# Kernel optimization log

Measured on AMD Instinct MI355X. Metric: run time of the kernel, lower is better.

Reference implementation:

```python
import jax, jax.numpy as jnp
import numpy as np

B, N, F = 1024, 784, 1
C1, C2, H, NCLS = 32, 32, 512, 10


def setup_inputs() -> dict:
    key = jax.random.key(0)
    ks = jax.random.split(key, 10)
    x = jax.random.normal(ks[0], (B, N, F), jnp.float32)
    # dense (renormalized-style) adjacency, shared across the batch; rows roughly sum to ~1
    a = jax.random.uniform(ks[1], (N, N), jnp.float32) * (2.0 / N)
    def glorot(k, shape):
        lim = np.sqrt(6.0 / (shape[0] + shape[1])).astype(np.float32)
        return jax.random.uniform(k, shape, jnp.float32, -lim, lim)
    return {
        "x": x,
        "a": a,
        "w1": glorot(ks[2], (F, C1)),
        "b1": jnp.zeros((C1,), jnp.float32),
        "w2": glorot(ks[3], (C1, C2)),
        "b2": jnp.zeros((C2,), jnp.float32),
        "wf1": glorot(ks[4], (N * C2, H)),
        "bf1": jnp.zeros((H,), jnp.float32),
        "wf2": glorot(ks[5], (H, NCLS)),
        "bf2": jnp.zeros((NCLS,), jnp.float32),
    }


def _graph_conv(x, a, w, b):
    # Spektral GraphConv (batch mode): elu(A @ (X @ W) + b)
    xw = jnp.einsum('bnf,fc->bnc', x, w)
    agg = jnp.einsum('nm,bmc->bnc', a, xw)
    return jax.nn.elu(agg + b)


def reference(x, a, w1, b1, w2, b2, wf1, bf1, wf2, bf2):
    h = _graph_conv(x, a, w1, b1)          # [B, N, 32]
    h = _graph_conv(h, a, w2, b2)          # [B, N, 32]
    h = h.reshape(h.shape[0], -1)          # Flatten -> [B, N*32]
    h = jax.nn.relu(h @ wf1 + bf1)         # [B, 512]
    return jax.nn.softmax(h @ wf2 + bf2, axis=-1)  # [B, 10]
```

## Files before the change

### kernel.cpp

```cpp
#include <hip/hip_runtime.h>
#include <hip/hip_bf16.h>
#include <math.h>

#define BATCH 1024
#define NREAL 784
#define NPAD  896
#define C1D   32
#define C2D   32
#define HDIM  512
#define NCLS  10
#define KFC   25088

#define KS_G1 7
#define KS_FC 14

#define BM 128
#define BN 128
#define BK 32

using bf16x8  = __attribute__((ext_vector_type(8))) __bf16;
using floatx4 = __attribute__((ext_vector_type(4))) float;

__device__ __forceinline__ float elu_f(float t) {
    return t > 0.f ? t : (__expf(t) - 1.f);
}

__device__ __forceinline__ void wg_barrier_lds() {
    asm volatile("s_waitcnt lgkmcnt(0)\n\ts_barrier" ::: "memory");
}

template<int MODE>
__launch_bounds__(256)
__global__ void gemm_bt(const __hip_bfloat16* __restrict__ A, int lda,
                        const __hip_bfloat16* __restrict__ Bm, int ldb,
                        int kIters, int kPerZ, size_t sliceStride,
                        float* __restrict__ outF, int ldc,
                        __hip_bfloat16* __restrict__ outH,
                        const float* __restrict__ bias)
{
    __shared__ __align__(16) __hip_bfloat16 As[2][BM * BK];
    __shared__ __align__(16) __hip_bfloat16 Bs[2][BN * BK];

    const int tid  = threadIdx.x;
    const int lane = tid & 63;
    const int wave = tid >> 6;
    const int wi = wave >> 1, wj = wave & 1;

    const int m0 = blockIdx.y * BM;
    const int n0 = blockIdx.x * BN;
    const int kBase = blockIdx.z * kPerZ;

    const int rowInChunk = lane >> 2;
    const int kOff8 = (lane & 3) * 8;

    const __hip_bfloat16* aSrc0 = A  + (size_t)(m0 + (wave * 2 + 0) * 16 + rowInChunk) * lda + kBase + kOff8;
    const __hip_bfloat16* aSrc1 = A  + (size_t)(m0 + (wave * 2 + 1) * 16 + rowInChunk) * lda + kBase + kOff8;
    const __hip_bfloat16* bSrc0 = Bm + (size_t)(n0 + (wave * 2 + 0) * 16 + rowInChunk) * ldb + kBase + kOff8;
    const __hip_bfloat16* bSrc1 = Bm + (size_t)(n0 + (wave * 2 + 1) * 16 + rowInChunk) * ldb + kBase + kOff8;

    const int wSlot = (((lane & 3) + ((lane >> 3) & 3)) & 3) * 8;
    const int ldsW0 = (wave * 2 + 0) * 512 + rowInChunk * 32 + wSlot;
    const int ldsW1 = ldsW0 + 512;

    const int rSlot = ((((lane >> 4) + (((lane & 15) >> 1) & 3)) & 3)) * 8;
    const int rRow  = lane & 15;

    floatx4 acc[4][4];
    const floatx4 zero4 = {0.f, 0.f, 0.f, 0.f};
    #pragma unroll
    for (int i = 0; i < 4; i++)
        #pragma unroll
        for (int j = 0; j < 4; j++) acc[i][j] = zero4;

    int4 aA0, aA1, bA0, bA1;
    int4 aB0, aB1, bB0, bB1;

    aA0 = *(const int4*)aSrc0; aA1 = *(const int4*)aSrc1;
    bA0 = *(const int4*)bSrc0; bA1 = *(const int4*)bSrc1;
    aSrc0 += BK; aSrc1 += BK; bSrc0 += BK; bSrc1 += BK;
    aB0 = *(const int4*)aSrc0; aB1 = *(const int4*)aSrc1;
    bB0 = *(const int4*)bSrc0; bB1 = *(const int4*)bSrc1;
    aSrc0 += BK; aSrc1 += BK; bSrc0 += BK; bSrc1 += BK;

    *(int4*)(&As[0][ldsW0]) = aA0;
    *(int4*)(&As[0][ldsW1]) = aA1;
    *(int4*)(&Bs[0][ldsW0]) = bA0;
    *(int4*)(&Bs[0][ldsW1]) = bA1;
    wg_barrier_lds();

    for (int kt = 0; kt < kIters; kt += 2) {
        const bool more = (kt + 2 < kIters);

        {
            bf16x8 af[4], bfr[4];
            #pragma unroll
            for (int mi = 0; mi < 4; mi++)
                af[mi] = *(const bf16x8*)(&As[0][(wi * 64 + mi * 16 + rRow) * BK + rSlot]);
            #pragma unroll
            for (int nj = 0; nj < 4; nj++)
                bfr[nj] = *(const bf16x8*)(&Bs[0][(wj * 64 + nj * 16 + rRow) * BK + rSlot]);

            if (more) {
                aA0 = *(const int4*)aSrc0; aA1 = *(const int4*)aSrc1;
                bA0 = *(const int4*)bSrc0; bA1 = *(const int4*)bSrc1;
                aSrc0 += BK; aSrc1 += BK; bSrc0 += BK; bSrc1 += BK;
            }
            *(int4*)(&As[1][ldsW0]) = aB0;
            *(int4*)(&As[1][ldsW1]) = aB1;
            *(int4*)(&Bs[1][ldsW0]) = bB0;
            *(int4*)(&Bs[1][ldsW1]) = bB1;

            #pragma unroll
            for (int mi = 0; mi < 4; mi++)
                #pragma unroll
                for (int nj = 0; nj < 4; nj++)
                    acc[mi][nj] = __builtin_amdgcn_mfma_f32_16x16x32_bf16(af[mi], bfr[nj], acc[mi][nj], 0, 0, 0);

            wg_barrier_lds();
        }

        {
            bf16x8 af[4], bfr[4];
            #pragma unroll
            for (int mi = 0; mi < 4; mi++)
                af[mi] = *(const bf16x8*)(&As[1][(wi * 64 + mi * 16 + rRow) * BK + rSlot]);
            #pragma unroll
            for (int nj = 0; nj < 4; nj++)
                bfr[nj] = *(const bf16x8*)(&Bs[1][(wj * 64 + nj * 16 + rRow) * BK + rSlot]);

            if (more) {
                aB0 = *(const int4*)aSrc0; aB1 = *(const int4*)aSrc1;
                bB0 = *(const int4*)bSrc0; bB1 = *(const int4*)bSrc1;
                aSrc0 += BK; aSrc1 += BK; bSrc0 += BK; bSrc1 += BK;
                *(int4*)(&As[0][ldsW0]) = aA0;
                *(int4*)(&As[0][ldsW1]) = aA1;
                *(int4*)(&Bs[0][ldsW0]) = bA0;
                *(int4*)(&Bs[0][ldsW1]) = bA1;
            }

            #pragma unroll
            for (int mi = 0; mi < 4; mi++)
                #pragma unroll
                for (int nj = 0; nj < 4; nj++)
                    acc[mi][nj] = __builtin_amdgcn_mfma_f32_16x16x32_bf16(af[mi], bfr[nj], acc[mi][nj], 0, 0, 0);

            wg_barrier_lds();
        }
    }

    #pragma unroll
    for (int mi = 0; mi < 4; mi++) {
        #pragma unroll
        for (int nj = 0; nj < 4; nj++) {
            #pragma unroll
            for (int r = 0; r < 4; r++) {
                const int row = m0 + wi * 64 + mi * 16 + (lane >> 4) * 4 + r;
                const int col = n0 + wj * 64 + nj * 16 + (lane & 15);
                const float v = acc[mi][nj][r];
                if (MODE == 1) {
                    if (row < NREAL) {
                        const int c = col & 31, b = col >> 5;
                        const float t = elu_f(v + bias[c]);
                        outH[(size_t)b * KFC + row * 32 + c] = __float2bfloat16(t);
                    }
                } else {
                    outF[(size_t)blockIdx.z * sliceStride + (size_t)row * ldc + col] = v;
                }
            }
        }
    }
}

__global__ void convX(const float* __restrict__ x, __hip_bfloat16* __restrict__ Xbf) {
    const int idx = blockIdx.x * 256 + threadIdx.x;
    if (idx >= BATCH * NPAD) return;
    const int m = idx % NPAD, b = idx / NPAD;
    const float v = (m < NREAL) ? x[(size_t)b * NREAL + m] : 0.f;
    Xbf[idx] = __float2bfloat16(v);
}

__global__ void convA(const float* __restrict__ a, __hip_bfloat16* __restrict__ Abf) {
    const int idx = blockIdx.x * 256 + threadIdx.x;
    if (idx >= NPAD * NPAD) return;
    const int m = idx % NPAD, n = idx / NPAD;
    const float v = (m < NREAL && n < NREAL) ? a[(size_t)n * NREAL + m] : 0.f;
    Abf[idx] = __float2bfloat16(v);
}

__global__ void convW(const float* __restrict__ wf1, __hip_bfloat16* __restrict__ Wt) {
    __shared__ float tile[32][33];
    const int k0 = blockIdx.x * 32, h0 = blockIdx.y * 32;
    const int tx = threadIdx.x, ty = threadIdx.y;
    #pragma unroll
    for (int i = 0; i < 4; i++)
        tile[ty * 4 + i][tx] = wf1[(size_t)(k0 + ty * 4 + i) * HDIM + h0 + tx];
    __syncthreads();
    #pragma unroll
    for (int i = 0; i < 4; i++)
        Wt[(size_t)(h0 + ty * 4 + i) * KFC + k0 + tx] = __float2bfloat16(tile[tx][ty * 4 + i]);
}

__global__ void layer1_fuse(const float* __restrict__ Ypart,
                            const float* __restrict__ w1, const float* __restrict__ b1,
                            const float* __restrict__ w2,
                            __hip_bfloat16* __restrict__ Tt)
{
    __shared__ __align__(16) float sW2[C1D * C2D];
    __shared__ float sw1[C1D], sb1[C1D];
    const int tid = threadIdx.x;
    for (int i = tid; i < C1D * C2D; i += 128) sW2[i] = w2[i];
    if (tid < C1D) { sw1[tid] = w1[tid]; sb1[tid] = b1[tid]; }
    __syncthreads();

    const int m = blockIdx.x * 128 + tid;
    const int b = blockIdx.y;
    float y = 0.f;
    #pragma unroll
    for (int z = 0; z < KS_G1; z++)
        y += Ypart[(size_t)z * (BATCH * NPAD) + (size_t)b * NPAD + m];

    float h[C1D];
    #pragma unroll
    for (int c1 = 0; c1 < C1D; c1++) h[c1] = elu_f(y * sw1[c1] + sb1[c1]);

    float4 t4[8];
    #pragma unroll
    for (int q = 0; q < 8; q++) t4[q] = make_float4(0.f, 0.f, 0.f, 0.f);
    #pragma unroll
    for (int c1 = 0; c1 < C1D; c1++) {
        const float hv = h[c1];
        const float4* row = (const float4*)(sW2 + c1 * C2D);
        #pragma unroll
        for (int q = 0; q < 8; q++) {
            const float4 w = row[q];
            t4[q].x += hv * w.x; t4[q].y += hv * w.y;
            t4[q].z += hv * w.z; t4[q].w += hv * w.w;
        }
    }
    const float* tf = (const float*)t4;
    #pragma unroll
    for (int c = 0; c < C2D; c++)
        Tt[((size_t)(b * 32 + c)) * NPAD + m] = __float2bfloat16(tf[c]);
}

__global__ void fc2_softmax(const float* __restrict__ part, const float* __restrict__ bf1,
                            const float* __restrict__ wf2, const float* __restrict__ bf2,
                            float* __restrict__ out)
{
    __shared__ float sW[HDIM * NCLS];
    __shared__ float sb[NCLS];
    const int tid = threadIdx.x;
    for (int i = tid; i < HDIM * NCLS; i += 256) sW[i] = wf2[i];
    if (tid < NCLS) sb[tid] = bf2[tid];
    __syncthreads();

    const int lane = tid & 63, wave = tid >> 6;
    const int b = blockIdx.x * 4 + wave;

    float acc[NCLS];
    #pragma unroll
    for (int c = 0; c < NCLS; c++) acc[c] = 0.f;
    #pragma unroll
    for (int q = 0; q < 8; q++) {
        const int h = q * 64 + lane;
        float hv = bf1[h];
        #pragma unroll
        for (int z = 0; z < KS_FC; z++)
            hv += part[(size_t)z * (BATCH * HDIM) + (size_t)b * HDIM + h];
        hv = hv > 0.f ? hv : 0.f;
        #pragma unroll
        for (int c = 0; c < NCLS; c++) acc[c] += hv * sW[h * NCLS + c];
    }
    #pragma unroll
    for (int c = 0; c < NCLS; c++) {
        #pragma unroll
        for (int off = 32; off >= 1; off >>= 1) acc[c] += __shfl_down(acc[c], off);
    }
    if (lane == 0) {
        float mx = -1e30f;
        #pragma unroll
        for (int c = 0; c < NCLS; c++) { acc[c] += sb[c]; mx = fmaxf(mx, acc[c]); }
        float e[NCLS], s = 0.f;
        #pragma unroll
        for (int c = 0; c < NCLS; c++) { e[c] = __expf(acc[c] - mx); s += e[c]; }
        const float inv = 1.f / s;
        #pragma unroll
        for (int c = 0; c < NCLS; c++) out[(size_t)b * NCLS + c] = e[c] * inv;
    }
}

extern "C" void kernel_launch(void* const* d_in, const int* in_sizes, int n_in,
                              void* d_out, int out_size, void* d_ws, size_t ws_size,
                              hipStream_t stream)
{
    const float* x   = (const float*)d_in[0];
    const float* a   = (const float*)d_in[1];
    const float* w1  = (const float*)d_in[2];
    const float* b1  = (const float*)d_in[3];
    const float* w2  = (const float*)d_in[4];
    const float* b2  = (const float*)d_in[5];
    const float* wf1 = (const float*)d_in[6];
    const float* bf1 = (const float*)d_in[7];
    const float* wf2 = (const float*)d_in[8];
    const float* bf2 = (const float*)d_in[9];
    float* out = (float*)d_out;

    char* ws = (char*)d_ws;
    __hip_bfloat16* h2f  = (__hip_bfloat16*)(ws + 0);
    float*          Ypart= (float*)(ws + 0);
    __hip_bfloat16* Tt   = (__hip_bfloat16*)(ws + 51380224);
    __hip_bfloat16* Wt   = (__hip_bfloat16*)(ws + 51380224);
    float*          part = (float*)(ws + 77070336);
    __hip_bfloat16* Abf  = (__hip_bfloat16*)(ws + 110100480);
    __hip_bfloat16* Xbf  = (__hip_bfloat16*)(ws + 111706112);

    convX<<<(BATCH * NPAD + 255) / 256, 256, 0, stream>>>(x, Xbf);
    convA<<<(NPAD * NPAD + 255) / 256, 256, 0, stream>>>(a, Abf);

    gemm_bt<2><<<dim3(NPAD / BN, BATCH / BM, KS_G1), 256, 0, stream>>>(
        Xbf, NPAD, Abf, NPAD, (NPAD / KS_G1) / BK, NPAD / KS_G1,
        (size_t)BATCH * NPAD, Ypart, NPAD, nullptr, nullptr);

    layer1_fuse<<<dim3(NPAD / 128, BATCH), 128, 0, stream>>>(Ypart, w1, b1, w2, Tt);

    gemm_bt<1><<<dim3((BATCH * 32) / BN, NPAD / BM, 1), 256, 0, stream>>>(
        Abf, NPAD, Tt, NPAD, NPAD / BK, 0, 0, nullptr, 0, h2f, b2);

    convW<<<dim3(KFC / 32, HDIM / 32), dim3(32, 8), 0, stream>>>(wf1, Wt);

    gemm_bt<2><<<dim3(HDIM / BN, BATCH / BM, KS_FC), 256, 0, stream>>>(
        h2f, KFC, Wt, KFC, (KFC / KS_FC) / BK, KFC / KS_FC,
        (size_t)BATCH * HDIM, part, HDIM, nullptr, nullptr);

    fc2_softmax<<<BATCH / 4, 256, 0, stream>>>(part, bf1, wf2, bf2, out);
}
```

Measured before the change: 300.1 us.

## Pre-swizzle A operands into MFMA fragment layout and load directly to registers

The A operand of every GEMM is now stored in a fragment-tiled layout (16 rows x 32 k chunks of 512 elements), so each wave loads its MFMA A fragments straight from global memory into registers and skips the LDS staging for A. A new prepXA kernel writes X and the adjacency into this layout. The layer-2 epilogue writes h2 in the same tiled layout for the FC GEMM. This halves LDS traffic and barrier-covered stores, at the cost of more register pressure, an extra copy of A, and less reuse of A across the waves that share it.

```diff
diff --git a/kernel.cpp b/kernel.cpp
--- a/kernel.cpp
+++ b/kernel.cpp
@@ -14,8 +14,6 @@
 #define KS_G1 7
 #define KS_FC 14
 
-#define BM 128
-#define BN 128
 #define BK 32
 
 using bf16x8  = __attribute__((ext_vector_type(8))) __bf16;
@@ -25,43 +23,46 @@
     return t > 0.f ? t : (__expf(t) - 1.f);
 }
 
+__device__ __forceinline__ bf16x8 ld8(const __hip_bfloat16* p) {
+    return *(const bf16x8*)p;
+}
+
 __device__ __forceinline__ void wg_barrier_lds() {
     asm volatile("s_waitcnt lgkmcnt(0)\n\ts_barrier" ::: "memory");
 }
 
+
 template<int MODE>
 __launch_bounds__(256)
-__global__ void gemm_bt(const __hip_bfloat16* __restrict__ A, int lda,
-                        const __hip_bfloat16* __restrict__ Bm, int ldb,
+__global__ void gemm_hy(const __hip_bfloat16* __restrict__ Af, int kcA,
+                        const __hip_bfloat16* __restrict__ Brow, int ldb,
                         int kIters, int kPerZ, size_t sliceStride,
                         float* __restrict__ outF, int ldc,
                         __hip_bfloat16* __restrict__ outH,
                         const float* __restrict__ bias)
 {
-    __shared__ __align__(16) __hip_bfloat16 As[2][BM * BK];
-    __shared__ __align__(16) __hip_bfloat16 Bs[2][BN * BK];
+    __shared__ __align__(16) __hip_bfloat16 Bs[2][128 * BK];
 
     const int tid  = threadIdx.x;
     const int lane = tid & 63;
     const int wave = tid >> 6;
     const int wi = wave >> 1, wj = wave & 1;
 
-    const int m0 = blockIdx.y * BM;
-    const int n0 = blockIdx.x * BN;
+    const int m0 = blockIdx.y * 128;
+    const int n0 = blockIdx.x * 128;
     const int kBase = blockIdx.z * kPerZ;
+
+    const __hip_bfloat16* aBase =
+        Af + ((size_t)(m0 / 16 + wi * 4) * kcA + (kBase >> 5)) * 512 + lane * 8;
+    const size_t aMi = (size_t)kcA * 512;
 
     const int rowInChunk = lane >> 2;
     const int kOff8 = (lane & 3) * 8;
-
-    const __hip_bfloat16* aSrc0 = A  + (size_t)(m0 + (wave * 2 + 0) * 16 + rowInChunk) * lda + kBase + kOff8;
-    const __hip_bfloat16* aSrc1 = A  + (size_t)(m0 + (wave * 2 + 1) * 16 + rowInChunk) * lda + kBase + kOff8;
-    const __hip_bfloat16* bSrc0 = Bm + (size_t)(n0 + (wave * 2 + 0) * 16 + rowInChunk) * ldb + kBase + kOff8;
-    const __hip_bfloat16* bSrc1 = Bm + (size_t)(n0 + (wave * 2 + 1) * 16 + rowInChunk) * ldb + kBase + kOff8;
-
+    const __hip_bfloat16* bSrc0 = Brow + (size_t)(n0 + (wave * 2 + 0) * 16 + rowInChunk) * ldb + kBase + kOff8;
+    const __hip_bfloat16* bSrc1 = Brow + (size_t)(n0 + (wave * 2 + 1) * 16 + rowInChunk) * ldb + kBase + kOff8;
     const int wSlot = (((lane & 3) + ((lane >> 3) & 3)) & 3) * 8;
     const int ldsW0 = (wave * 2 + 0) * 512 + rowInChunk * 32 + wSlot;
     const int ldsW1 = ldsW0 + 512;
-
     const int rSlot = ((((lane >> 4) + (((lane & 15) >> 1) & 3)) & 3)) * 8;
     const int rRow  = lane & 15;
 
@@ -72,77 +73,71 @@
         #pragma unroll
         for (int j = 0; j < 4; j++) acc[i][j] = zero4;
 
-    int4 aA0, aA1, bA0, bA1;
-    int4 aB0, aB1, bB0, bB1;
-
-    aA0 = *(const int4*)aSrc0; aA1 = *(const int4*)aSrc1;
-    bA0 = *(const int4*)bSrc0; bA1 = *(const int4*)bSrc1;
-    aSrc0 += BK; aSrc1 += BK; bSrc0 += BK; bSrc1 += BK;
-    aB0 = *(const int4*)aSrc0; aB1 = *(const int4*)aSrc1;
-    bB0 = *(const int4*)bSrc0; bB1 = *(const int4*)bSrc1;
-    aSrc0 += BK; aSrc1 += BK; bSrc0 += BK; bSrc1 += BK;
-
-    *(int4*)(&As[0][ldsW0]) = aA0;
-    *(int4*)(&As[0][ldsW1]) = aA1;
-    *(int4*)(&Bs[0][ldsW0]) = bA0;
-    *(int4*)(&Bs[0][ldsW1]) = bA1;
+    bf16x8 aFe[4], aFo[4];
+    int4 bRe0, bRe1, bRo0, bRo1;
+
+    #pragma unroll
+    for (int mi = 0; mi < 4; mi++) aFe[mi] = ld8(aBase + mi * aMi);
+    bRe0 = *(const int4*)bSrc0; bRe1 = *(const int4*)bSrc1;
+    bSrc0 += BK; bSrc1 += BK;
+    #pragma unroll
+    for (int mi = 0; mi < 4; mi++) aFo[mi] = ld8(aBase + mi * aMi + 512);
+    bRo0 = *(const int4*)bSrc0; bRo1 = *(const int4*)bSrc1;
+    bSrc0 += BK; bSrc1 += BK;
+
+    *(int4*)(&Bs[0][ldsW0]) = bRe0;
+    *(int4*)(&Bs[0][ldsW1]) = bRe1;
     wg_barrier_lds();
 
     for (int kt = 0; kt < kIters; kt += 2) {
         const bool more = (kt + 2 < kIters);
 
         {
-            bf16x8 af[4], bfr[4];
-            #pragma unroll
-            for (int mi = 0; mi < 4; mi++)
-                af[mi] = *(const bf16x8*)(&As[0][(wi * 64 + mi * 16 + rRow) * BK + rSlot]);
+            bf16x8 bfr[4];
             #pragma unroll
             for (int nj = 0; nj < 4; nj++)
-                bfr[nj] = *(const bf16x8*)(&Bs[0][(wj * 64 + nj * 16 + rRow) * BK + rSlot]);
-
-            if (more) {
-                aA0 = *(const int4*)aSrc0; aA1 = *(const int4*)aSrc1;
-                bA0 = *(const int4*)bSrc0; bA1 = *(const int4*)bSrc1;
-                aSrc0 += BK; aSrc1 += BK; bSrc0 += BK; bSrc1 += BK;
-            }
-            *(int4*)(&As[1][ldsW0]) = aB0;
-            *(int4*)(&As[1][ldsW1]) = aB1;
-            *(int4*)(&Bs[1][ldsW0]) = bB0;
-            *(int4*)(&Bs[1][ldsW1]) = bB1;
+                bfr[nj] = *(const bf16x8*)(&Bs[0][((wj * 4 + nj) * 16 + rRow) * BK + rSlot]);
 
             #pragma unroll
             for (int mi = 0; mi < 4; mi++)
                 #pragma unroll
                 for (int nj = 0; nj < 4; nj++)
-                    acc[mi][nj] = __builtin_amdgcn_mfma_f32_16x16x32_bf16(af[mi], bfr[nj], acc[mi][nj], 0, 0, 0);
+                    acc[mi][nj] = __builtin_amdgcn_mfma_f32_16x16x32_bf16(aFe[mi], bfr[nj], acc[mi][nj], 0, 0, 0);
+
+            if (more) {
+                #pragma unroll
+                for (int mi = 0; mi < 4; mi++)
+                    aFe[mi] = ld8(aBase + mi * aMi + (size_t)(kt + 2) * 512);
+                bRe0 = *(const int4*)bSrc0; bRe1 = *(const int4*)bSrc1;
+                bSrc0 += BK; bSrc1 += BK;
+            }
+            *(int4*)(&Bs[1][ldsW0]) = bRo0;
+            *(int4*)(&Bs[1][ldsW1]) = bRo1;
 
             wg_barrier_lds();
         }
 
         {
-            bf16x8 af[4], bfr[4];
-            #pragma unroll
-            for (int mi = 0; mi < 4; mi++)
-                af[mi] = *(const bf16x8*)(&As[1][(wi * 64 + mi * 16 + rRow) * BK + rSlot]);
+            bf16x8 bfr[4];
             #pragma unroll
             for (int nj = 0; nj < 4; nj++)
-                bfr[nj] = *(const bf16x8*)(&Bs[1][(wj * 64 + nj * 16 + rRow) * BK + rSlot]);
-
-            if (more) {
-                aB0 = *(const int4*)aSrc0; aB1 = *(const int4*)aSrc1;
-                bB0 = *(const int4*)bSrc0; bB1 = *(const int4*)bSrc1;
-                aSrc0 += BK; aSrc1 += BK; bSrc0 += BK; bSrc1 += BK;
-                *(int4*)(&As[0][ldsW0]) = aA0;
-                *(int4*)(&As[0][ldsW1]) = aA1;
-                *(int4*)(&Bs[0][ldsW0]) = bA0;
-                *(int4*)(&Bs[0][ldsW1]) = bA1;
-            }
+                bfr[nj] = *(const bf16x8*)(&Bs[1][((wj * 4 + nj) * 16 + rRow) * BK + rSlot]);
 
             #pragma unroll
             for (int mi = 0; mi < 4; mi++)
                 #pragma unroll
                 for (int nj = 0; nj < 4; nj++)
-                    acc[mi][nj] = __builtin_amdgcn_mfma_f32_16x16x32_bf16(af[mi], bfr[nj], acc[mi][nj], 0, 0, 0);
+                    acc[mi][nj] = __builtin_amdgcn_mfma_f32_16x16x32_bf16(aFo[mi], bfr[nj], acc[mi][nj], 0, 0, 0);
+
+            if (more) {
+                #pragma unroll
+                for (int mi = 0; mi < 4; mi++)
+                    aFo[mi] = ld8(aBase + mi * aMi + (size_t)(kt + 3) * 512);
+                bRo0 = *(const int4*)bSrc0; bRo1 = *(const int4*)bSrc1;
+                bSrc0 += BK; bSrc1 += BK;
+                *(int4*)(&Bs[0][ldsW0]) = bRe0;
+                *(int4*)(&Bs[0][ldsW1]) = bRe1;
+            }
 
             wg_barrier_lds();
         }
@@ -154,37 +149,61 @@
         for (int nj = 0; nj < 4; nj++) {
             #pragma unroll
             for (int r = 0; r < 4; r++) {
-                const int row = m0 + wi * 64 + mi * 16 + (lane >> 4) * 4 + r;
-                const int col = n0 + wj * 64 + nj * 16 + (lane & 15);
+                const int orow = m0 + wi * 64 + mi * 16 + (lane >> 4) * 4 + r;
+                const int ocol = n0 + wj * 64 + nj * 16 + (lane & 15);
                 const float v = acc[mi][nj][r];
                 if (MODE == 1) {
-                    if (row < NREAL) {
-                        const int c = col & 31, b = col >> 5;
+                    if (orow < NREAL) {
+                        const int b = ocol >> 5, c = ocol & 31;
                         const float t = elu_f(v + bias[c]);
-                        outH[(size_t)b * KFC + row * 32 + c] = __float2bfloat16(t);
+                        const size_t ad = ((size_t)(b >> 4) * 784 + orow) * 512
+                                        + (c >> 3) * 128 + (b & 15) * 8 + (c & 7);
+                        outH[ad] = __float2bfloat16(t);
                     }
                 } else {
-                    outF[(size_t)blockIdx.z * sliceStride + (size_t)row * ldc + col] = v;
+                    outF[(size_t)blockIdx.z * sliceStride + (size_t)orow * ldc + ocol] = v;
                 }
             }
         }
     }
 }
 
-__global__ void convX(const float* __restrict__ x, __hip_bfloat16* __restrict__ Xbf) {
-    const int idx = blockIdx.x * 256 + threadIdx.x;
-    if (idx >= BATCH * NPAD) return;
-    const int m = idx % NPAD, b = idx / NPAD;
-    const float v = (m < NREAL) ? x[(size_t)b * NREAL + m] : 0.f;
-    Xbf[idx] = __float2bfloat16(v);
-}
-
-__global__ void convA(const float* __restrict__ a, __hip_bfloat16* __restrict__ Abf) {
+__global__ void prepXA(const float* __restrict__ x, const float* __restrict__ a,
+                       __hip_bfloat16* __restrict__ Xf, __hip_bfloat16* __restrict__ Af)
+{
+    const int XC = (BATCH / 16) * (NPAD / 32);
+    int t = blockIdx.x * 256 + threadIdx.x;
+    const float* src;
+    __hip_bfloat16* dst;
+    int chunk, L, rowsValid;
+    if (t < XC * 64) {
+        chunk = t >> 6; L = t & 63; src = x; dst = Xf; rowsValid = BATCH;
+    } else {
+        t -= XC * 64; chunk = t >> 6; L = t & 63; src = a; dst = Af; rowsValid = NREAL;
+    }
+    const int row = (chunk / 28) * 16 + (L & 15);
+    const int k0  = ((chunk % 28) * 4 + (L >> 4)) * 8;
+    __hip_bfloat16 o[8];
+    if (k0 < NREAL && row < rowsValid) {
+        const float4* p = (const float4*)(src + (size_t)row * NREAL + k0);
+        const float4 lo = p[0], hi = p[1];
+        o[0] = __float2bfloat16(lo.x); o[1] = __float2bfloat16(lo.y);
+        o[2] = __float2bfloat16(lo.z); o[3] = __float2bfloat16(lo.w);
+        o[4] = __float2bfloat16(hi.x); o[5] = __float2bfloat16(hi.y);
+        o[6] = __float2bfloat16(hi.z); o[7] = __float2bfloat16(hi.w);
+    } else {
+        #pragma unroll
+        for (int j = 0; j < 8; j++) o[j] = __float2bfloat16(0.f);
+    }
+    *(int4*)(dst + (size_t)chunk * 512 + L * 8) = *(const int4*)o;
+}
+
+__global__ void convA(const float* __restrict__ a, __hip_bfloat16* __restrict__ Ar) {
     const int idx = blockIdx.x * 256 + threadIdx.x;
     if (idx >= NPAD * NPAD) return;
     const int m = idx % NPAD, n = idx / NPAD;
     const float v = (m < NREAL && n < NREAL) ? a[(size_t)n * NREAL + m] : 0.f;
-    Abf[idx] = __float2bfloat16(v);
+    Ar[idx] = __float2bfloat16(v);
 }
 
 __global__ void convW(const float* __restrict__ wf1, __hip_bfloat16* __restrict__ Wt) {
@@ -311,25 +330,26 @@
     __hip_bfloat16* Tt   = (__hip_bfloat16*)(ws + 51380224);
     __hip_bfloat16* Wt   = (__hip_bfloat16*)(ws + 51380224);
     float*          part = (float*)(ws + 77070336);
-    __hip_bfloat16* Abf  = (__hip_bfloat16*)(ws + 110100480);
-    __hip_bfloat16* Xbf  = (__hip_bfloat16*)(ws + 111706112);
-
-    convX<<<(BATCH * NPAD + 255) / 256, 256, 0, stream>>>(x, Xbf);
-    convA<<<(NPAD * NPAD + 255) / 256, 256, 0, stream>>>(a, Abf);
-
-    gemm_bt<2><<<dim3(NPAD / BN, BATCH / BM, KS_G1), 256, 0, stream>>>(
-        Xbf, NPAD, Abf, NPAD, (NPAD / KS_G1) / BK, NPAD / KS_G1,
+    __hip_bfloat16* Af   = (__hip_bfloat16*)(ws + 110100480);
+    __hip_bfloat16* Xf   = (__hip_bfloat16*)(ws + 111706112);
+    __hip_bfloat16* Ar   = (__hip_bfloat16*)(ws + 113541120);
+
+    prepXA<<<840, 256, 0, stream>>>(x, a, Xf, Af);
+    convA<<<(NPAD * NPAD + 255) / 256, 256, 0, stream>>>(a, Ar);
+
+    gemm_hy<2><<<dim3(NPAD / 128, BATCH / 128, KS_G1), 256, 0, stream>>>(
+        Xf, 28, Ar, NPAD, (NPAD / KS_G1) / BK, NPAD / KS_G1,
         (size_t)BATCH * NPAD, Ypart, NPAD, nullptr, nullptr);
 
     layer1_fuse<<<dim3(NPAD / 128, BATCH), 128, 0, stream>>>(Ypart, w1, b1, w2, Tt);
 
-    gemm_bt<1><<<dim3((BATCH * 32) / BN, NPAD / BM, 1), 256, 0, stream>>>(
-        Abf, NPAD, Tt, NPAD, NPAD / BK, 0, 0, nullptr, 0, h2f, b2);
+    gemm_hy<1><<<dim3((BATCH * 32) / 128, NPAD / 128, 1), 256, 0, stream>>>(
+        Af, 28, Tt, NPAD, NPAD / BK, 0, 0, nullptr, 0, h2f, b2);
 
     convW<<<dim3(KFC / 32, HDIM / 32), dim3(32, 8), 0, stream>>>(wf1, Wt);
 
-    gemm_bt<2><<<dim3(HDIM / BN, BATCH / BM, KS_FC), 256, 0, stream>>>(
-        h2f, KFC, Wt, KFC, (KFC / KS_FC) / BK, KFC / KS_FC,
+    gemm_hy<2><<<dim3(HDIM / 128, BATCH / 128, KS_FC), 256, 0, stream>>>(
+        h2f, 784, Wt, KFC, (KFC / KS_FC) / BK, KFC / KS_FC,
         (size_t)BATCH * HDIM, part, HDIM, nullptr, nullptr);
 
     fc2_softmax<<<BATCH / 4, 256, 0, stream>>>(part, bf1, wf2, bf2, out);
```

After: 319.8 us. +6.6%, slower.

## Fuse first graph-conv GEMM with layer-1 epilogue and merge conversion kernels

Applied to the files above, without the earlier changes.

Replaces the split-K first aggregation GEMM, which wrote seven fp32 partial slices, and the separate layer1_fuse kernel with one kernel. That kernel computes a 64x64 tile over the full K, stages it in LDS, and applies the ELU plus W2 projection before writing Tt. This removes the large fp32 partial buffer traffic and one launch. The X and A conversion kernels are also merged into a single launch. In exchange the new GEMM uses smaller tiles with a full-K loop, and each thread does a heavy scalar epilogue.

```diff
diff --git a/kernel.cpp b/kernel.cpp
--- a/kernel.cpp
+++ b/kernel.cpp
@@ -11,11 +11,9 @@
 #define NCLS  10
 #define KFC   25088
 
-#define KS_G1 7
 #define KS_FC 14
-
-#define BM 128
-#define BN 128
+#define G1_ITERS 28
+
 #define BK 32
 
 using bf16x8  = __attribute__((ext_vector_type(8))) __bf16;
@@ -38,16 +36,16 @@
                         __hip_bfloat16* __restrict__ outH,
                         const float* __restrict__ bias)
 {
-    __shared__ __align__(16) __hip_bfloat16 As[2][BM * BK];
-    __shared__ __align__(16) __hip_bfloat16 Bs[2][BN * BK];
+    __shared__ __align__(16) __hip_bfloat16 As[2][128 * BK];
+    __shared__ __align__(16) __hip_bfloat16 Bs[2][128 * BK];
 
     const int tid  = threadIdx.x;
     const int lane = tid & 63;
     const int wave = tid >> 6;
     const int wi = wave >> 1, wj = wave & 1;
 
-    const int m0 = blockIdx.y * BM;
-    const int n0 = blockIdx.x * BN;
+    const int m0 = blockIdx.y * 128;
+    const int n0 = blockIdx.x * 128;
     const int kBase = blockIdx.z * kPerZ;
 
     const int rowInChunk = lane >> 2;
@@ -72,20 +70,20 @@
         #pragma unroll
         for (int j = 0; j < 4; j++) acc[i][j] = zero4;
 
-    int4 aA0, aA1, bA0, bA1;
-    int4 aB0, aB1, bB0, bB1;
-
-    aA0 = *(const int4*)aSrc0; aA1 = *(const int4*)aSrc1;
-    bA0 = *(const int4*)bSrc0; bA1 = *(const int4*)bSrc1;
+    int4 aAe0, aAe1, bAe0, bAe1;
+    int4 aAo0, aAo1, bAo0, bAo1;
+
+    aAe0 = *(const int4*)aSrc0; aAe1 = *(const int4*)aSrc1;
+    bAe0 = *(const int4*)bSrc0; bAe1 = *(const int4*)bSrc1;
     aSrc0 += BK; aSrc1 += BK; bSrc0 += BK; bSrc1 += BK;
-    aB0 = *(const int4*)aSrc0; aB1 = *(const int4*)aSrc1;
-    bB0 = *(const int4*)bSrc0; bB1 = *(const int4*)bSrc1;
+    aAo0 = *(const int4*)aSrc0; aAo1 = *(const int4*)aSrc1;
+    bAo0 = *(const int4*)bSrc0; bAo1 = *(const int4*)bSrc1;
     aSrc0 += BK; aSrc1 += BK; bSrc0 += BK; bSrc1 += BK;
 
-    *(int4*)(&As[0][ldsW0]) = aA0;
-    *(int4*)(&As[0][ldsW1]) = aA1;
-    *(int4*)(&Bs[0][ldsW0]) = bA0;
-    *(int4*)(&Bs[0][ldsW1]) = bA1;
+    *(int4*)(&As[0][ldsW0]) = aAe0;
+    *(int4*)(&As[0][ldsW1]) = aAe1;
+    *(int4*)(&Bs[0][ldsW0]) = bAe0;
+    *(int4*)(&Bs[0][ldsW1]) = bAe1;
     wg_barrier_lds();
 
     for (int kt = 0; kt < kIters; kt += 2) {
@@ -101,14 +99,14 @@
                 bfr[nj] = *(const bf16x8*)(&Bs[0][(wj * 64 + nj * 16 + rRow) * BK + rSlot]);
 
             if (more) {
-                aA0 = *(const int4*)aSrc0; aA1 = *(const int4*)aSrc1;
-                bA0 = *(const int4*)bSrc0; bA1 = *(const int4*)bSrc1;
+                aAe0 = *(const int4*)aSrc0; aAe1 = *(const int4*)aSrc1;
+                bAe0 = *(const int4*)bSrc0; bAe1 = *(const int4*)bSrc1;
                 aSrc0 += BK; aSrc1 += BK; bSrc0 += BK; bSrc1 += BK;
             }
-            *(int4*)(&As[1][ldsW0]) = aB0;
-            *(int4*)(&As[1][ldsW1]) = aB1;
-            *(int4*)(&Bs[1][ldsW0]) = bB0;
-            *(int4*)(&Bs[1][ldsW1]) = bB1;
+            *(int4*)(&As[1][ldsW0]) = aAo0;
+            *(int4*)(&As[1][ldsW1]) = aAo1;
+            *(int4*)(&Bs[1][ldsW0]) = bAo0;
+            *(int4*)(&Bs[1][ldsW1]) = bAo1;
 
             #pragma unroll
             for (int mi = 0; mi < 4; mi++)
@@ -129,13 +127,13 @@
                 bfr[nj] = *(const bf16x8*)(&Bs[1][(wj * 64 + nj * 16 + rRow) * BK + rSlot]);
 
             if (more) {
-                aB0 = *(const int4*)aSrc0; aB1 = *(const int4*)aSrc1;
-                bB0 = *(const int4*)bSrc0; bB1 = *(const int4*)bSrc1;
+                aAo0 = *(const int4*)aSrc0; aAo1 = *(const int4*)aSrc1;
+                bAo0 = *(const int4*)bSrc0; bAo1 = *(const int4*)bSrc1;
                 aSrc0 += BK; aSrc1 += BK; bSrc0 += BK; bSrc1 += BK;
-                *(int4*)(&As[0][ldsW0]) = aA0;
-                *(int4*)(&As[0][ldsW1]) = aA1;
-                *(int4*)(&Bs[0][ldsW0]) = bA0;
-                *(int4*)(&Bs[0][ldsW1]) = bA1;
+                *(int4*)(&As[0][ldsW0]) = aAe0;
+                *(int4*)(&As[0][ldsW1]) = aAe1;
+                *(int4*)(&Bs[0][ldsW0]) = bAe0;
+                *(int4*)(&Bs[0][ldsW1]) = bAe1;
             }
 
             #pragma unroll
@@ -171,20 +169,154 @@
     }
 }
 
-__global__ void convX(const float* __restrict__ x, __hip_bfloat16* __restrict__ Xbf) {
-    const int idx = blockIdx.x * 256 + threadIdx.x;
-    if (idx >= BATCH * NPAD) return;
-    const int m = idx % NPAD, b = idx / NPAD;
-    const float v = (m < NREAL) ? x[(size_t)b * NREAL + m] : 0.f;
-    Xbf[idx] = __float2bfloat16(v);
-}
-
-__global__ void convA(const float* __restrict__ a, __hip_bfloat16* __restrict__ Abf) {
-    const int idx = blockIdx.x * 256 + threadIdx.x;
-    if (idx >= NPAD * NPAD) return;
-    const int m = idx % NPAD, n = idx / NPAD;
-    const float v = (m < NREAL && n < NREAL) ? a[(size_t)n * NREAL + m] : 0.f;
-    Abf[idx] = __float2bfloat16(v);
+__launch_bounds__(256)
+__global__ void g1_layer1(const __hip_bfloat16* __restrict__ Xbf,
+                          const __hip_bfloat16* __restrict__ Ar,
+                          const float* __restrict__ w1, const float* __restrict__ b1,
+                          const float* __restrict__ w2,
+                          __hip_bfloat16* __restrict__ Tt)
+{
+    __shared__ __align__(16) __hip_bfloat16 As[2][64 * BK];
+    __shared__ __align__(16) __hip_bfloat16 Bs[2][64 * BK];
+    __shared__ float Ys[64 * 65];
+    __shared__ __align__(16) float sW2[C1D * C2D];
+    __shared__ float sw1[C1D], sb1[C1D];
+
+    const int tid  = threadIdx.x;
+    const int lane = tid & 63;
+    const int wave = tid >> 6;
+    const int wi = wave >> 1, wj = wave & 1;
+
+    const int n0 = blockIdx.x * 64;
+    const int m0 = blockIdx.y * 64;
+
+    for (int i = tid; i < C1D * C2D; i += 256) sW2[i] = w2[i];
+    if (tid < C1D) { sw1[tid] = w1[tid]; sb1[tid] = b1[tid]; }
+
+    const int rowInChunk = lane >> 2;
+    const int kOff8 = (lane & 3) * 8;
+    const __hip_bfloat16* aSrc = Xbf + (size_t)(m0 + wave * 16 + rowInChunk) * NPAD + kOff8;
+    const __hip_bfloat16* bSrc = Ar  + (size_t)(n0 + wave * 16 + rowInChunk) * NPAD + kOff8;
+
+    const int wSlot = (((lane & 3) + ((lane >> 3) & 3)) & 3) * 8;
+    const int ldsW = wave * 512 + rowInChunk * 32 + wSlot;
+    const int rSlot = ((((lane >> 4) + (((lane & 15) >> 1) & 3)) & 3)) * 8;
+    const int rRow  = lane & 15;
+
+    floatx4 acc[2][2];
+    const floatx4 zero4 = {0.f, 0.f, 0.f, 0.f};
+    #pragma unroll
+    for (int i = 0; i < 2; i++)
+        #pragma unroll
+        for (int j = 0; j < 2; j++) acc[i][j] = zero4;
+
+    int4 aE, bE, aO, bO;
+    aE = *(const int4*)aSrc; bE = *(const int4*)bSrc; aSrc += BK; bSrc += BK;
+    aO = *(const int4*)aSrc; bO = *(const int4*)bSrc; aSrc += BK; bSrc += BK;
+
+    *(int4*)(&As[0][ldsW]) = aE;
+    *(int4*)(&Bs[0][ldsW]) = bE;
+    wg_barrier_lds();
+
+    for (int kt = 0; kt < G1_ITERS; kt += 2) {
+        const bool more = (kt + 2 < G1_ITERS);
+        {
+            bf16x8 af[2], bfr[2];
+            #pragma unroll
+            for (int mi = 0; mi < 2; mi++)
+                af[mi] = *(const bf16x8*)(&As[0][(wi * 32 + mi * 16 + rRow) * BK + rSlot]);
+            #pragma unroll
+            for (int nj = 0; nj < 2; nj++)
+                bfr[nj] = *(const bf16x8*)(&Bs[0][(wj * 32 + nj * 16 + rRow) * BK + rSlot]);
+            if (more) { aE = *(const int4*)aSrc; bE = *(const int4*)bSrc; aSrc += BK; bSrc += BK; }
+            *(int4*)(&As[1][ldsW]) = aO;
+            *(int4*)(&Bs[1][ldsW]) = bO;
+            #pragma unroll
+            for (int mi = 0; mi < 2; mi++)
+                #pragma unroll
+                for (int nj = 0; nj < 2; nj++)
+                    acc[mi][nj] = __builtin_amdgcn_mfma_f32_16x16x32_bf16(af[mi], bfr[nj], acc[mi][nj], 0, 0, 0);
+            wg_barrier_lds();
+        }
+        {
+            bf16x8 af[2], bfr[2];
+            #pragma unroll
+            for (int mi = 0; mi < 2; mi++)
+                af[mi] = *(const bf16x8*)(&As[1][(wi * 32 + mi * 16 + rRow) * BK + rSlot]);
+            #pragma unroll
+            for (int nj = 0; nj < 2; nj++)
+                bfr[nj] = *(const bf16x8*)(&Bs[1][(wj * 32 + nj * 16 + rRow) * BK + rSlot]);
+            if (more) {
+                aO = *(const int4*)aSrc; bO = *(const int4*)bSrc; aSrc += BK; bSrc += BK;
+                *(int4*)(&As[0][ldsW]) = aE;
+                *(int4*)(&Bs[0][ldsW]) = bE;
+            }
+            #pragma unroll
+            for (int mi = 0; mi < 2; mi++)
+                #pragma unroll
+                for (int nj = 0; nj < 2; nj++)
+                    acc[mi][nj] = __builtin_amdgcn_mfma_f32_16x16x32_bf16(af[mi], bfr[nj], acc[mi][nj], 0, 0, 0);
+            wg_barrier_lds();
+        }
+    }
+
+    #pragma unroll
+    for (int mi = 0; mi < 2; mi++)
+        #pragma unroll
+        for (int nj = 0; nj < 2; nj++)
+            #pragma unroll
+            for (int r = 0; r < 4; r++) {
+                const int bl = wi * 32 + mi * 16 + (lane >> 4) * 4 + r;
+                const int nl = wj * 32 + nj * 16 + (lane & 15);
+                Ys[bl * 65 + nl] = acc[mi][nj][r];
+            }
+    __syncthreads();
+
+    const int n_l = (tid & 31) * 2;
+    const int bq  = tid >> 5;
+    #pragma unroll 1
+    for (int i = 0; i < 8; i++) {
+        const int bl = bq * 8 + i;
+        const float y0 = Ys[bl * 65 + n_l];
+        const float y1 = Ys[bl * 65 + n_l + 1];
+        float t0[C2D], t1[C2D];
+        #pragma unroll
+        for (int c = 0; c < C2D; c++) { t0[c] = 0.f; t1[c] = 0.f; }
+        #pragma unroll
+        for (int c1 = 0; c1 < C1D; c1++) {
+            const float h0 = elu_f(y0 * sw1[c1] + sb1[c1]);
+            const float h1 = elu_f(y1 * sw1[c1] + sb1[c1]);
+            const float* wr = sW2 + c1 * C2D;
+            #pragma unroll
+            for (int c = 0; c < C2D; c++) { t0[c] += h0 * wr[c]; t1[c] += h1 * wr[c]; }
+        }
+        const int bg = m0 + bl;
+        #pragma unroll
+        for (int c = 0; c < C2D; c++) {
+            __hip_bfloat162 pv;
+            pv.x = __float2bfloat16(t0[c]);
+            pv.y = __float2bfloat16(t1[c]);
+            *(__hip_bfloat162*)(Tt + (size_t)(bg * 32 + c) * NPAD + n0 + n_l) = pv;
+        }
+    }
+}
+
+__global__ void convXA(const float* __restrict__ x, const float* __restrict__ a,
+                       __hip_bfloat16* __restrict__ Xbf, __hip_bfloat16* __restrict__ Ar)
+{
+    int idx = blockIdx.x * 256 + threadIdx.x;
+    if (idx < BATCH * NPAD) {
+        const int m = idx % NPAD, b = idx / NPAD;
+        const float v = (m < NREAL) ? x[(size_t)b * NREAL + m] : 0.f;
+        Xbf[idx] = __float2bfloat16(v);
+    } else {
+        idx -= BATCH * NPAD;
+        if (idx < NPAD * NPAD) {
+            const int m = idx % NPAD, n = idx / NPAD;
+            const float v = (m < NREAL && n < NREAL) ? a[(size_t)n * NREAL + m] : 0.f;
+            Ar[idx] = __float2bfloat16(v);
+        }
+    }
 }
 
 __global__ void convW(const float* __restrict__ wf1, __hip_bfloat16* __restrict__ Wt) {
@@ -198,49 +330,6 @@
     #pragma unroll
     for (int i = 0; i < 4; i++)
         Wt[(size_t)(h0 + ty * 4 + i) * KFC + k0 + tx] = __float2bfloat16(tile[tx][ty * 4 + i]);
-}
-
-__global__ void layer1_fuse(const float* __restrict__ Ypart,
-                            const float* __restrict__ w1, const float* __restrict__ b1,
-                            const float* __restrict__ w2,
-                            __hip_bfloat16* __restrict__ Tt)
-{
-    __shared__ __align__(16) float sW2[C1D * C2D];
-    __shared__ float sw1[C1D], sb1[C1D];
-    const int tid = threadIdx.x;
-    for (int i = tid; i < C1D * C2D; i += 128) sW2[i] = w2[i];
-    if (tid < C1D) { sw1[tid] = w1[tid]; sb1[tid] = b1[tid]; }
-    __syncthreads();
-
-    const int m = blockIdx.x * 128 + tid;
-    const int b = blockIdx.y;
-    float y = 0.f;
-    #pragma unroll
-    for (int z = 0; z < KS_G1; z++)
-        y += Ypart[(size_t)z * (BATCH * NPAD) + (size_t)b * NPAD + m];
-
-    float h[C1D];
-    #pragma unroll
-    for (int c1 = 0; c1 < C1D; c1++) h[c1] = elu_f(y * sw1[c1] + sb1[c1]);
-
-    float4 t4[8];
-    #pragma unroll
-    for (int q = 0; q < 8; q++) t4[q] = make_float4(0.f, 0.f, 0.f, 0.f);
-    #pragma unroll
-    for (int c1 = 0; c1 < C1D; c1++) {
-        const float hv = h[c1];
-        const float4* row = (const float4*)(sW2 + c1 * C2D);
-        #pragma unroll
-        for (int q = 0; q < 8; q++) {
-            const float4 w = row[q];
-            t4[q].x += hv * w.x; t4[q].y += hv * w.y;
-            t4[q].z += hv * w.z; t4[q].w += hv * w.w;
-        }
-    }
-    const float* tf = (const float*)t4;
-    #pragma unroll
-    for (int c = 0; c < C2D; c++)
-        Tt[((size_t)(b * 32 + c)) * NPAD + m] = __float2bfloat16(tf[c]);
 }
 
 __global__ void fc2_softmax(const float* __restrict__ part, const float* __restrict__ bf1,
@@ -307,28 +396,22 @@
 
     char* ws = (char*)d_ws;
     __hip_bfloat16* h2f  = (__hip_bfloat16*)(ws + 0);
-    float*          Ypart= (float*)(ws + 0);
     __hip_bfloat16* Tt   = (__hip_bfloat16*)(ws + 51380224);
     __hip_bfloat16* Wt   = (__hip_bfloat16*)(ws + 51380224);
     float*          part = (float*)(ws + 77070336);
-    __hip_bfloat16* Abf  = (__hip_bfloat16*)(ws + 110100480);
+    __hip_bfloat16* Ar   = (__hip_bfloat16*)(ws + 110100480);
     __hip_bfloat16* Xbf  = (__hip_bfloat16*)(ws + 111706112);
 
-    convX<<<(BATCH * NPAD + 255) / 256, 256, 0, stream>>>(x, Xbf);
-    convA<<<(NPAD * NPAD + 255) / 256, 256, 0, stream>>>(a, Abf);
-
-    gemm_bt<2><<<dim3(NPAD / BN, BATCH / BM, KS_G1), 256, 0, stream>>>(
-        Xbf, NPAD, Abf, NPAD, (NPAD / KS_G1) / BK, NPAD / KS_G1,
-        (size_t)BATCH * NPAD, Ypart, NPAD, nullptr, nullptr);
-
-    layer1_fuse<<<dim3(NPAD / 128, BATCH), 128, 0, stream>>>(Ypart, w1, b1, w2, Tt);
-
-    gemm_bt<1><<<dim3((BATCH * 32) / BN, NPAD / BM, 1), 256, 0, stream>>>(
-        Abf, NPAD, Tt, NPAD, NPAD / BK, 0, 0, nullptr, 0, h2f, b2);
+    convXA<<<(BATCH * NPAD + NPAD * NPAD + 255) / 256, 256, 0, stream>>>(x, a, Xbf, Ar);
+
+    g1_layer1<<<dim3(NPAD / 64, BATCH / 64), 256, 0, stream>>>(Xbf, Ar, w1, b1, w2, Tt);
+
+    gemm_bt<1><<<dim3((BATCH * 32) / 128, NPAD / 128, 1), 256, 0, stream>>>(
+        Ar, NPAD, Tt, NPAD, NPAD / BK, 0, 0, nullptr, 0, h2f, b2);
 
     convW<<<dim3(KFC / 32, HDIM / 32), dim3(32, 8), 0, stream>>>(wf1, Wt);
 
-    gemm_bt<2><<<dim3(HDIM / BN, BATCH / BM, KS_FC), 256, 0, stream>>>(
+    gemm_bt<2><<<dim3(HDIM / 128, BATCH / 128, KS_FC), 256, 0, stream>>>(
         h2f, KFC, Wt, KFC, (KFC / KS_FC) / BK, KFC / KS_FC,
         (size_t)BATCH * HDIM, part, HDIM, nullptr, nullptr);
 
```

Result: slower. 579.9 us (+93.2%).
